# Kernel optimization log

Hardware: AMD Instinct MI355X
Metric: run time of the kernel (lower is better)

## Reference

```python
import jax, jax.numpy as jnp
import numpy as np

N_QUBITS = 12
DIM = 2 ** N_QUBITS
N_RES_LAYERS = 3
N_HEADS = 2
N_ATTN_LAYERS = 2
SEQ_LEN = 64
HORIZON = 4
BATCH = 8
N_PARAMS = N_QUBITS * 2 * N_ATTN_LAYERS  # 48
FEAT = N_QUBITS * N_HEADS  # 24

# ---- static (numpy) precomputed gate structures (little-endian, qiskit convention) ----
_idx = np.arange(DIM)

def _cx_perm(c, t):
    # CNOT: flip target bit where control bit is 1 -> index permutation
    return np.where(((_idx >> c) & 1) == 1, _idx ^ (1 << t), _idx)

def _cz_phase(a, b):
    return (1.0 - 2.0 * (((_idx >> a) & 1) * ((_idx >> b) & 1))).astype(np.float32)

CX_LADDER = [jnp.asarray(_cx_perm(i, i + 1)) for i in range(N_QUBITS - 1)]
CX_RING = jnp.asarray(_cx_perm(N_QUBITS - 1, 0))
CX_LONG = jnp.asarray(_cx_perm(0, N_QUBITS - 1))
_CZ = []
for _layer in range(N_RES_LAYERS):
    _ph = np.ones(DIM, np.float32)
    for _i in range(_layer % 2, N_QUBITS - 1, 2):
        _ph *= _cz_phase(_i, _i + 1)
    _CZ.append(jnp.asarray(_ph))
# Qiskit Pauli label 'I'*i + 'Z' + 'I'*(n-i-1) acts on qubit n-1-i (big-endian labels)
Z_SIGNS = jnp.asarray(np.stack([
    (1.0 - 2.0 * ((_idx >> (N_QUBITS - 1 - i)) & 1)).astype(np.float32)
    for i in range(N_QUBITS)]))  # (n, DIM)


def _apply_1q(state, gate, q):
    # state: (..., DIM); gate: (2,2) or (...,2,2) broadcastable against leading dims
    hi = DIM >> (q + 1)
    lo = 1 << q
    s = state.reshape(state.shape[:-1] + (hi, 2, lo))
    out = jnp.einsum('...ij,...hjl->...hil', gate, s)
    return out.reshape(state.shape)


def _ry(theta):
    c = jnp.cos(theta / 2)
    s = jnp.sin(theta / 2)
    g = jnp.stack([jnp.stack([c, -s], -1), jnp.stack([s, c], -1)], -2)
    return g.astype(jnp.complex64)


def _rz(phi):
    em = jnp.exp(-0.5j * phi)
    ep = jnp.exp(0.5j * phi)
    z = jnp.zeros_like(em)
    return jnp.stack([jnp.stack([em, z], -1), jnp.stack([z, ep], -1)], -2)


def _u3(t, p, l):
    ct = jnp.cos(t / 2).astype(jnp.complex64)
    st = jnp.sin(t / 2).astype(jnp.complex64)
    return jnp.stack([jnp.stack([ct, -jnp.exp(1j * l) * st]),
                      jnp.stack([jnp.exp(1j * p) * st, jnp.exp(1j * (p + l)) * ct])])


def _encode_reservoir(x, res_params):
    # x: (B,T) normalized scalars -> batched statevectors (B,T,DIM)
    B, T = x.shape
    # H^{\otimes n} |0...0> = uniform superposition
    state = jnp.full((B, T, DIM), 1.0 / np.sqrt(DIM), jnp.complex64)
    for i in range(N_QUBITS):
        state = _apply_1q(state, _ry(x * np.pi * (i + 1) / N_QUBITS), i)
        state = _apply_1q(state, _rz(x * np.pi / (i + 1)), i)
    for p in CX_LADDER:
        state = state[..., p]
    state = state[..., CX_RING]
    # fixed random reservoir
    for layer in range(N_RES_LAYERS):
        for i in range(N_QUBITS):
            g = _u3(res_params[layer, i, 0], res_params[layer, i, 1], res_params[layer, i, 2])
            state = _apply_1q(state, g, i)
        state = state * _CZ[layer]
        state = state[..., CX_LONG]  # n > 2
    return state


def _project(state, params):
    # projection circuit: per layer RY/RZ on each qubit then CNOT ladder; then <Z_i>
    for layer in range(N_ATTN_LAYERS):
        for i in range(N_QUBITS):
            k = (layer * N_QUBITS + i) * 2
            state = _apply_1q(state, _ry(params[k]), i)
            state = _apply_1q(state, _rz(params[k + 1]), i)
        for p in CX_LADDER:
            state = state[..., p]
    probs = state.real ** 2 + state.imag ** 2  # (B,T,DIM)
    return jnp.einsum('btd,qd->btq', probs, Z_SIGNS)  # (B,T,n)


def setup_inputs() -> dict:
    key = jax.random.key(0)
    ks = jax.random.split(key, 6)
    sequence = jax.random.uniform(ks[0], (BATCH, SEQ_LEN), jnp.float32)
    res_params = jax.random.uniform(ks[1], (N_RES_LAYERS, N_QUBITS, 3), jnp.float32,
                                    minval=0.0, maxval=2.0 * np.pi)
    head_params = jax.random.uniform(ks[2], (N_HEADS, 3, N_PARAMS), jnp.float32,
                                     minval=0.0, maxval=2.0 * np.pi)
    W1 = jax.random.normal(ks[3], (FEAT, 2 * FEAT), jnp.float32) / np.sqrt(FEAT)
    b1 = jnp.zeros((2 * FEAT,), jnp.float32)
    W2 = jax.random.normal(ks[4], (2 * FEAT, HORIZON), jnp.float32) / np.sqrt(2 * FEAT)
    b2 = jnp.zeros((HORIZON,), jnp.float32)
    return {'sequence': sequence, 'res_params': res_params, 'head_params': head_params,
            'W1': W1, 'b1': b1, 'W2': W2, 'b2': b2}


def reference(sequence, res_params, head_params, W1, b1, W2, b2):
    states = _encode_reservoir(sequence, res_params)  # (B,T,DIM)
    T = sequence.shape[1]
    mask = jnp.triu(jnp.full((T, T), -1e9, jnp.float32), k=1)
    outs = []
    for h in range(N_HEADS):
        Q = _project(states, head_params[h, 0])
        K = _project(states, head_params[h, 1])
        V = _project(states, head_params[h, 2])
        scores = jnp.einsum('btd,bsd->bts', Q, K) / np.sqrt(N_QUBITS) + mask
        attn = jax.nn.softmax(scores, axis=-1)
        outs.append(jnp.einsum('bts,bsd->btd', attn, V))
    feats = jnp.concatenate(outs, -1)  # (B,T,FEAT)
    last = feats[:, -1, :]
    hdn = jax.nn.gelu(last @ W1 + b1, approximate=False)  # torch GELU default = exact erf
    pred = hdn @ W2 + b2  # (B, HORIZON)
    return pred
```

## Files before the change

### kernel.cpp

```cpp
#include <hip/hip_runtime.h>
#include <hip/hip_bf16.h>


#define PADDED 4224

__device__ __forceinline__ int PD(int j) { return j + (j >> 5); }

__device__ __forceinline__ int mapIdx(int j, int mode) {
  if (mode == 1) { int k = j ^ ((j >> 11) & 1); return k ^ ((k & 0x7FF) << 1); }
  if (mode == 2) { return j ^ ((j & 1) << 11); }
  if (mode == 3) { return j ^ ((j & 0x7FF) << 1); }
  return j;
}

template <int L>
__device__ __forceinline__ int layoutIdx(int tid, int r) {
  if constexpr (L == 0) return (tid << 4) | r;
  else if constexpr (L == 1) return ((tid & 0xF0) << 4) | (r << 4) | (tid & 15);
  else return (r << 8) | tid;
}

template <int L>
__device__ __forceinline__ void ldsRead16(const float* sR, const float* sI, int tid, int mode,
                                          float ar[16], float ai[16]) {
#pragma unroll
  for (int r = 0; r < 16; ++r) {
    int j = layoutIdx<L>(tid, r);
    int a = PD(mapIdx(j, mode));
    ar[r] = sR[a]; ai[r] = sI[a];
  }
}

template <int L>
__device__ __forceinline__ void ldsWrite16(float* sR, float* sI, int tid,
                                           const float ar[16], const float ai[16], int czmask) {
#pragma unroll
  for (int r = 0; r < 16; ++r) {
    int j = layoutIdx<L>(tid, r);
    float vr = ar[r], vi = ai[r];
    if (czmask) {
      float sg = (__popc((j & (j >> 1)) & czmask) & 1) ? -1.0f : 1.0f;
      vr *= sg; vi *= sg;
    }
    int a = PD(j);
    sR[a] = vr; sI[a] = vi;
  }
}

__device__ __forceinline__ void applyU34(float ar[16], float ai[16], const float (*ut)[8]) {
#pragma unroll
  for (int b = 0; b < 4; ++b) {
    const float* u = ut[b];
    float u00r = u[0], u00i = u[1], u01r = u[2], u01i = u[3];
    float u10r = u[4], u10i = u[5], u11r = u[6], u11i = u[7];
#pragma unroll
    for (int m = 0; m < 8; ++m) {
      int p0 = ((m >> b) << (b + 1)) | (m & ((1 << b) - 1));
      int p1 = p0 | (1 << b);
      float x0r = ar[p0], x0i = ai[p0], x1r = ar[p1], x1i = ai[p1];
      ar[p0] = u00r * x0r - u00i * x0i + u01r * x1r - u01i * x1i;
      ai[p0] = u00r * x0i + u00i * x0r + u01r * x1i + u01i * x1r;
      ar[p1] = u10r * x0r - u10i * x0i + u11r * x1r - u11i * x1i;
      ai[p1] = u10r * x0i + u10i * x0r + u11r * x1i + u11i * x1r;
    }
  }
}

__device__ __forceinline__ void applyRyRz4(float ar[16], float ai[16], const float4* gt) {
#pragma unroll
  for (int b = 0; b < 4; ++b) {
    float4 g = gt[b];
    float c = g.x, s = g.y, zr = g.z, zi = g.w;
#pragma unroll
    for (int m = 0; m < 8; ++m) {
      int p0 = ((m >> b) << (b + 1)) | (m & ((1 << b) - 1));
      int p1 = p0 | (1 << b);
      float n0r = c * ar[p0] - s * ar[p1];
      float n0i = c * ai[p0] - s * ai[p1];
      float n1r = s * ar[p0] + c * ar[p1];
      float n1i = s * ai[p0] + c * ai[p1];
      ar[p0] = n0r * zr + n0i * zi;  ai[p0] = n0i * zr - n0r * zi;
      ar[p1] = n1r * zr - n1i * zi;  ai[p1] = n1i * zr + n1r * zi;
    }
  }
}

template <int L>
__device__ __forceinline__ void encPass(float* sR, float* sI, int tid, int mode,
                                        const float (*ut)[8], int czmask) {
  float ar[16], ai[16];
  ldsRead16<L>(sR, sI, tid, mode, ar, ai);
  if (mode != 0) __syncthreads();
  applyU34(ar, ai, ut);
  ldsWrite16<L>(sR, sI, tid, ar, ai, czmask);
  __syncthreads();
}

template <int L>
__device__ __forceinline__ void projPass(float* sR, float* sI, int tid, int mode, const float4* gt) {
  float ar[16], ai[16];
  ldsRead16<L>(sR, sI, tid, mode, ar, ai);
  if (mode != 0) __syncthreads();
  applyRyRz4(ar, ai, gt);
  ldsWrite16<L>(sR, sI, tid, ar, ai, 0);
  __syncthreads();
}

__device__ __forceinline__ void projFinal(const float* sR, const float* sI, int tid,
                                          const float4* gt, float feat[12]) {
  float ar[16], ai[16];
#pragma unroll
  for (int r = 0; r < 16; ++r) {
    int a = PD((r << 8) | tid);
    ar[r] = sR[a]; ai[r] = sI[a];
  }
  applyRyRz4(ar, ai, gt);
  float sp = 0.f, f0 = 0.f, f1 = 0.f, f2 = 0.f, f3 = 0.f;
  int pt = __popc(tid) & 1;
#pragma unroll
  for (int r = 0; r < 16; ++r) {
    float p = ar[r] * ar[r] + ai[r] * ai[r];
    sp += p;
    int tr = r ^ (r << 1); tr ^= (tr << 2);
    f0 += ((pt ^ ((tr >> 3) & 1)) ? -p : p);
    f1 += ((pt ^ ((tr >> 2) & 1)) ? -p : p);
    f2 += ((pt ^ ((tr >> 1) & 1)) ? -p : p);
    f3 += ((pt ^ (tr & 1)) ? -p : p);
  }
  feat[0] = f0; feat[1] = f1; feat[2] = f2; feat[3] = f3;
  int tt = tid ^ (tid << 1); tt ^= (tt << 2); tt ^= (tt << 4);
#pragma unroll
  for (int q = 4; q < 12; ++q)
    feat[q] = ((tt >> (11 - q)) & 1) ? -sp : sp;
}

__device__ __forceinline__ float waveReduce(float v) {
#pragma unroll
  for (int off = 32; off; off >>= 1) v += __shfl_xor(v, off, 64);
  return v;
}

__global__ __launch_bounds__(256, 2) void qstates_kernel(
    const float* __restrict__ seq, const float* __restrict__ resp,
    const float* __restrict__ hparams, float* __restrict__ ws) {
  __shared__ float sRe[PADDED], sIm[PADDED];
  __shared__ float4 qtab[12];
  __shared__ float utab[36][8];
  __shared__ float4 ptab[24];
  __shared__ float red[4][12];

  const int tid = threadIdx.x;
  const int blk = blockIdx.x;
  const int b = blk >> 6;
  const int t = blk & 63;
  const float x = seq[(b << 6) | t];
  const float PI = 3.14159265358979323846f;
  const float RS2 = 0.70710678118654752440f;

  if (tid < 12) {
    int i = tid;
    float th = x * PI * (float)(i + 1) / 12.0f;
    float ph = x * PI / (float)(i + 1);
    float s, c;  sincosf(0.5f * th, &s, &c);
    float zi, zr; sincosf(0.5f * ph, &zi, &zr);
    float k0 = (c - s) * RS2, k1 = (c + s) * RS2;
    qtab[i] = make_float4(k0 * zr, -k0 * zi, k1 * zr, k1 * zi);
  }
  if (tid >= 64 && tid < 100) {
    int i = tid - 64;
    const float* rp = resp + i * 3;
    float st, ct;  sincosf(0.5f * rp[0], &st, &ct);
    float sp2, cp; sincosf(rp[1], &sp2, &cp);
    float sl, cl;  sincosf(rp[2], &sl, &cl);
    float spl, cpl; sincosf(rp[1] + rp[2], &spl, &cpl);
    float* u = utab[i];
    u[0] = ct;       u[1] = 0.0f;
    u[2] = -cl * st; u[3] = -sl * st;
    u[4] = cp * st;  u[5] = sp2 * st;
    u[6] = cpl * ct; u[7] = spl * ct;
  }
  __syncthreads();

  {
    float pr, pi;
    {
      float4 g = qtab[4];
      int sb = tid & 1;
      pr = sb ? g.z : g.x; pi = sb ? g.w : g.y;
    }
#pragma unroll
    for (int q = 5; q < 12; ++q) {
      float4 g = qtab[q];
      int sb = (tid >> (q - 4)) & 1;
      float fr = sb ? g.z : g.x, fi = sb ? g.w : g.y;
      float nr = pr * fr - pi * fi;
      pi = pr * fi + pi * fr; pr = nr;
    }
    float4 g0 = qtab[0], g1 = qtab[1], g2 = qtab[2], g3 = qtab[3];
    float c01r[4], c01i[4], c23r[4], c23i[4];
#pragma unroll
    for (int i2 = 0; i2 < 4; ++i2) {
      float f0r = (i2 & 1) ? g0.z : g0.x, f0i = (i2 & 1) ? g0.w : g0.y;
      float f1r = (i2 & 2) ? g1.z : g1.x, f1i = (i2 & 2) ? g1.w : g1.y;
      c01r[i2] = f0r * f1r - f0i * f1i; c01i[i2] = f0r * f1i + f0i * f1r;
      float f2r = (i2 & 1) ? g2.z : g2.x, f2i = (i2 & 1) ? g2.w : g2.y;
      float f3r = (i2 & 2) ? g3.z : g3.x, f3i = (i2 & 2) ? g3.w : g3.y;
      c23r[i2] = f2r * f3r - f2i * f3i; c23i[i2] = f2r * f3i + f2i * f3r;
    }
#pragma unroll
    for (int r = 0; r < 16; ++r) {
      float lr = c01r[r & 3] * c23r[r >> 2] - c01i[r & 3] * c23i[r >> 2];
      float li = c01r[r & 3] * c23i[r >> 2] + c01i[r & 3] * c23r[r >> 2];
      int a = PD((tid << 4) | r);
      sRe[a] = pr * lr - pi * li;
      sIm[a] = pr * li + pi * lr;
    }
  }
  __syncthreads();

  for (int l = 0; l < 3; ++l) {
    int czm = (l & 1) ? 0x2AA : 0x555;
    encPass<0>(sRe, sIm, tid, (l == 0) ? 1 : 2, &utab[l * 12], 0);
    encPass<1>(sRe, sIm, tid, 0, &utab[l * 12 + 4], 0);
    encPass<2>(sRe, sIm, tid, 0, &utab[l * 12 + 8], czm);
  }

  float encR[16], encI[16];
#pragma unroll
  for (int r = 0; r < 16; ++r) {
    int j = (tid << 4) | r;
    int a = PD(j ^ ((j & 1) << 11));
    encR[r] = sRe[a]; encI[r] = sIm[a];
  }

  float* wsK = ws;
  float* wsV = ws + 12288;
  float* wsQ = ws + 24576;

  const int nproj = (t == 63) ? 6 : 4;
  for (int pj = 0; pj < nproj; ++pj) {
    int h, which;
    if (pj < 4) { h = pj >> 1; which = (pj & 1) ? 2 : 1; }
    else        { h = pj - 4;  which = 0; }
    const float* hp = hparams + (h * 3 + which) * 48;
    if (tid < 24) {
      int k = tid * 2;
      float s, c;  sincosf(0.5f * hp[k], &s, &c);
      float zi, zr; sincosf(0.5f * hp[k + 1], &zi, &zr);
      ptab[tid] = make_float4(c, s, zr, zi);
    }
    __syncthreads();

    {
      float ar[16], ai[16];
#pragma unroll
      for (int r = 0; r < 16; ++r) { ar[r] = encR[r]; ai[r] = encI[r]; }
      applyRyRz4(ar, ai, &ptab[0]);
      ldsWrite16<0>(sRe, sIm, tid, ar, ai, 0);
      __syncthreads();
    }
    projPass<1>(sRe, sIm, tid, 0, &ptab[4]);
    projPass<2>(sRe, sIm, tid, 0, &ptab[8]);
    projPass<0>(sRe, sIm, tid, 3, &ptab[12]);
    projPass<1>(sRe, sIm, tid, 0, &ptab[16]);

    float feat[12];
    projFinal(sRe, sIm, tid, &ptab[20], feat);
#pragma unroll
    for (int q = 0; q < 12; ++q) feat[q] = waveReduce(feat[q]);
    int wid = tid >> 6;
    if ((tid & 63) == 0) {
#pragma unroll
      for (int q = 0; q < 12; ++q) red[wid][q] = feat[q];
    }
    __syncthreads();
    if (tid < 12) {
      float v = red[0][tid] + red[1][tid] + red[2][tid] + red[3][tid];
      float* dst;
      if (which == 1)      dst = wsK + (((h << 3) + b) * 64 + t) * 12;
      else if (which == 2) dst = wsV + (((h << 3) + b) * 64 + t) * 12;
      else                 dst = wsQ + ((h << 3) + b) * 12;
      dst[tid] = v;
    }
    __syncthreads();
  }
}

__global__ __launch_bounds__(64) void qhead_kernel(
    const float* __restrict__ ws,
    const float* __restrict__ W1, const float* __restrict__ b1,
    const float* __restrict__ W2, const float* __restrict__ b2,
    float* __restrict__ out) {
  __shared__ float feats[24];
  __shared__ float hdn[48];
  const int b = blockIdx.x;
  const int lane = threadIdx.x;
  const float* Kf = ws;
  const float* Vf = ws + 12288;
  const float* Qf = ws + 24576;
  for (int h = 0; h < 2; ++h) {
    const float* q  = Qf + ((h << 3) + b) * 12;
    const float* kr = Kf + ((((h << 3) + b) << 6) + lane) * 12;
    float dot = 0.f;
#pragma unroll
    for (int d = 0; d < 12; ++d) dot += q[d] * kr[d];
    dot *= 0.288675134594812882f;
    float mx = dot;
#pragma unroll
    for (int off = 32; off; off >>= 1) mx = fmaxf(mx, __shfl_xor(mx, off, 64));
    float e = expf(dot - mx);
    float se = e;
#pragma unroll
    for (int off = 32; off; off >>= 1) se += __shfl_xor(se, off, 64);
    float a = e / se;
    const float* vr = Vf + ((((h << 3) + b) << 6) + lane) * 12;
#pragma unroll
    for (int d = 0; d < 12; ++d) {
      float v = a * vr[d];
#pragma unroll
      for (int off = 32; off; off >>= 1) v += __shfl_xor(v, off, 64);
      if (lane == 0) feats[h * 12 + d] = v;
    }
  }
  __syncthreads();
  if (lane < 48) {
    float acc = b1[lane];
#pragma unroll
    for (int f = 0; f < 24; ++f) acc += feats[f] * W1[f * 48 + lane];
    hdn[lane] = 0.5f * acc * (1.0f + erff(acc * 0.70710678118654752440f));
  }
  __syncthreads();
  if (lane < 4) {
    float acc = b2[lane];
#pragma unroll
    for (int k = 0; k < 48; ++k) acc += hdn[k] * W2[k * 4 + lane];
    out[(b << 2) | lane] = acc;
  }
}

extern "C" void kernel_launch(void* const* d_in, const int* in_sizes, int n_in,
                              void* d_out, int out_size, void* d_ws, size_t ws_size,
                              hipStream_t stream) {
  const float* seq     = (const float*)d_in[0];
  const float* resp    = (const float*)d_in[1];
  const float* hparams = (const float*)d_in[2];
  const float* W1      = (const float*)d_in[3];
  const float* b1      = (const float*)d_in[4];
  const float* W2      = (const float*)d_in[5];
  const float* b2      = (const float*)d_in[6];
  float* out = (float*)d_out;
  float* ws  = (float*)d_ws;

  hipLaunchKernelGGL(qstates_kernel, dim3(512), dim3(256), 0, stream, seq, resp, hparams, ws);
  hipLaunchKernelGGL(qhead_kernel, dim3(8), dim3(64), 0, stream, ws, W1, b1, W2, b2, out);
}
```

Measured before the change: 182.9 us.

## Split encoder and projections into separate kernels to parallelize projections

The fused per-timestep kernel is split in two. An encoder kernel writes each encoded statevector to workspace, and a projection kernel launches one block per (timestep, head, Q/K/V) projection, 2064 blocks instead of 512, so the serial per-block projection loop is spread across the GPU. Gate math is also trimmed: the known-zero u00 imaginary term is dropped from U3, and RZ is applied as a relative phase on the |1> amplitude only. That phase-only form relies on global phase not affecting the Z expectation values. The split path needs about 16 MB of workspace for the statevector round trip through global memory, and it falls back to the monolithic kernel when the workspace is too small.

```diff
diff --git a/kernel.cpp b/kernel.cpp
--- a/kernel.cpp
+++ b/kernel.cpp
@@ -51,15 +51,16 @@
 #pragma unroll
   for (int b = 0; b < 4; ++b) {
     const float* u = ut[b];
-    float u00r = u[0], u00i = u[1], u01r = u[2], u01i = u[3];
+    float u00r = u[0];
+    float u01r = u[2], u01i = u[3];
     float u10r = u[4], u10i = u[5], u11r = u[6], u11i = u[7];
 #pragma unroll
     for (int m = 0; m < 8; ++m) {
       int p0 = ((m >> b) << (b + 1)) | (m & ((1 << b) - 1));
       int p1 = p0 | (1 << b);
       float x0r = ar[p0], x0i = ai[p0], x1r = ar[p1], x1i = ai[p1];
-      ar[p0] = u00r * x0r - u00i * x0i + u01r * x1r - u01i * x1i;
-      ai[p0] = u00r * x0i + u00i * x0r + u01r * x1i + u01i * x1r;
+      ar[p0] = u00r * x0r + u01r * x1r - u01i * x1i;
+      ai[p0] = u00r * x0i + u01r * x1i + u01i * x1r;
       ar[p1] = u10r * x0r - u10i * x0i + u11r * x1r - u11i * x1i;
       ai[p1] = u10r * x0i + u10i * x0r + u11r * x1i + u11i * x1r;
     }
@@ -75,12 +76,13 @@
     for (int m = 0; m < 8; ++m) {
       int p0 = ((m >> b) << (b + 1)) | (m & ((1 << b) - 1));
       int p1 = p0 | (1 << b);
-      float n0r = c * ar[p0] - s * ar[p1];
-      float n0i = c * ai[p0] - s * ai[p1];
-      float n1r = s * ar[p0] + c * ar[p1];
-      float n1i = s * ai[p0] + c * ai[p1];
-      ar[p0] = n0r * zr + n0i * zi;  ai[p0] = n0i * zr - n0r * zi;
-      ar[p1] = n1r * zr - n1i * zi;  ai[p1] = n1i * zr + n1r * zi;
+      float x0r = ar[p0], x0i = ai[p0], x1r = ar[p1], x1i = ai[p1];
+      float n0r = c * x0r - s * x1r;
+      float n0i = c * x0i - s * x1i;
+      float wr  = s * x0r + c * x1r;
+      float wi  = s * x0i + c * x1i;
+      ar[p0] = n0r;              ai[p0] = n0i;
+      ar[p1] = wr * zr - wi * zi; ai[p1] = wr * zi + wi * zr;
     }
   }
 }
@@ -140,23 +142,10 @@
   return v;
 }
 
-__global__ __launch_bounds__(256, 2) void qstates_kernel(
-    const float* __restrict__ seq, const float* __restrict__ resp,
-    const float* __restrict__ hparams, float* __restrict__ ws) {
-  __shared__ float sRe[PADDED], sIm[PADDED];
-  __shared__ float4 qtab[12];
-  __shared__ float utab[36][8];
-  __shared__ float4 ptab[24];
-  __shared__ float red[4][12];
-
-  const int tid = threadIdx.x;
-  const int blk = blockIdx.x;
-  const int b = blk >> 6;
-  const int t = blk & 63;
-  const float x = seq[(b << 6) | t];
+
+__device__ __forceinline__ void buildQtab(float4* qtab, int tid, float x) {
   const float PI = 3.14159265358979323846f;
   const float RS2 = 0.70710678118654752440f;
-
   if (tid < 12) {
     int i = tid;
     float th = x * PI * (float)(i + 1) / 12.0f;
@@ -166,6 +155,9 @@
     float k0 = (c - s) * RS2, k1 = (c + s) * RS2;
     qtab[i] = make_float4(k0 * zr, -k0 * zi, k1 * zr, k1 * zi);
   }
+}
+
+__device__ __forceinline__ void buildUtab(float (*utab)[8], int tid, const float* resp) {
   if (tid >= 64 && tid < 100) {
     int i = tid - 64;
     const float* rp = resp + i * 3;
@@ -179,43 +171,174 @@
     u[4] = cp * st;  u[5] = sp2 * st;
     u[6] = cpl * ct; u[7] = spl * ct;
   }
-  __syncthreads();
-
+}
+
+__device__ __forceinline__ void initProduct(float* sRe, float* sIm, int tid, const float4* qtab) {
+  float pr, pi;
   {
-    float pr, pi;
-    {
-      float4 g = qtab[4];
-      int sb = tid & 1;
-      pr = sb ? g.z : g.x; pi = sb ? g.w : g.y;
-    }
-#pragma unroll
-    for (int q = 5; q < 12; ++q) {
-      float4 g = qtab[q];
-      int sb = (tid >> (q - 4)) & 1;
-      float fr = sb ? g.z : g.x, fi = sb ? g.w : g.y;
-      float nr = pr * fr - pi * fi;
-      pi = pr * fi + pi * fr; pr = nr;
-    }
-    float4 g0 = qtab[0], g1 = qtab[1], g2 = qtab[2], g3 = qtab[3];
-    float c01r[4], c01i[4], c23r[4], c23i[4];
-#pragma unroll
-    for (int i2 = 0; i2 < 4; ++i2) {
-      float f0r = (i2 & 1) ? g0.z : g0.x, f0i = (i2 & 1) ? g0.w : g0.y;
-      float f1r = (i2 & 2) ? g1.z : g1.x, f1i = (i2 & 2) ? g1.w : g1.y;
-      c01r[i2] = f0r * f1r - f0i * f1i; c01i[i2] = f0r * f1i + f0i * f1r;
-      float f2r = (i2 & 1) ? g2.z : g2.x, f2i = (i2 & 1) ? g2.w : g2.y;
-      float f3r = (i2 & 2) ? g3.z : g3.x, f3i = (i2 & 2) ? g3.w : g3.y;
-      c23r[i2] = f2r * f3r - f2i * f3i; c23i[i2] = f2r * f3i + f2i * f3r;
-    }
+    float4 g = qtab[4];
+    int sb = tid & 1;
+    pr = sb ? g.z : g.x; pi = sb ? g.w : g.y;
+  }
+#pragma unroll
+  for (int q = 5; q < 12; ++q) {
+    float4 g = qtab[q];
+    int sb = (tid >> (q - 4)) & 1;
+    float fr = sb ? g.z : g.x, fi = sb ? g.w : g.y;
+    float nr = pr * fr - pi * fi;
+    pi = pr * fi + pi * fr; pr = nr;
+  }
+  float4 g0 = qtab[0], g1 = qtab[1], g2 = qtab[2], g3 = qtab[3];
+  float c01r[4], c01i[4], c23r[4], c23i[4];
+#pragma unroll
+  for (int i2 = 0; i2 < 4; ++i2) {
+    float f0r = (i2 & 1) ? g0.z : g0.x, f0i = (i2 & 1) ? g0.w : g0.y;
+    float f1r = (i2 & 2) ? g1.z : g1.x, f1i = (i2 & 2) ? g1.w : g1.y;
+    c01r[i2] = f0r * f1r - f0i * f1i; c01i[i2] = f0r * f1i + f0i * f1r;
+    float f2r = (i2 & 1) ? g2.z : g2.x, f2i = (i2 & 1) ? g2.w : g2.y;
+    float f3r = (i2 & 2) ? g3.z : g3.x, f3i = (i2 & 2) ? g3.w : g3.y;
+    c23r[i2] = f2r * f3r - f2i * f3i; c23i[i2] = f2r * f3i + f2i * f3r;
+  }
+#pragma unroll
+  for (int r = 0; r < 16; ++r) {
+    float lr = c01r[r & 3] * c23r[r >> 2] - c01i[r & 3] * c23i[r >> 2];
+    float li = c01r[r & 3] * c23i[r >> 2] + c01i[r & 3] * c23r[r >> 2];
+    int a = PD((tid << 4) | r);
+    sRe[a] = pr * lr - pi * li;
+    sIm[a] = pr * li + pi * lr;
+  }
+}
+
+__device__ __forceinline__ void buildPtab(float4* ptab, int tid, const float* hp) {
+  if (tid < 24) {
+    int k = tid * 2;
+    float s, c;  sincosf(0.5f * hp[k], &s, &c);
+    float zi, zr; sincosf(hp[k + 1], &zi, &zr);
+    ptab[tid] = make_float4(c, s, zr, zi);
+  }
+}
+
+
+__global__ __launch_bounds__(256, 2) void enc_kernel(
+    const float* __restrict__ seq, const float* __restrict__ resp,
+    float* __restrict__ wsStates) {
+  __shared__ float sRe[PADDED], sIm[PADDED];
+  __shared__ float4 qtab[12];
+  __shared__ float utab[36][8];
+
+  const int tid = threadIdx.x;
+  const int blk = blockIdx.x;
+  const float x = seq[blk];
+
+  buildQtab(qtab, tid, x);
+  buildUtab(utab, tid, resp);
+  __syncthreads();
+
+  initProduct(sRe, sIm, tid, qtab);
+  __syncthreads();
+
+  encPass<0>(sRe, sIm, tid, 1, &utab[0], 0);
+  encPass<1>(sRe, sIm, tid, 0, &utab[4], 0);
+  encPass<2>(sRe, sIm, tid, 0, &utab[8], 0x555);
+  encPass<0>(sRe, sIm, tid, 2, &utab[12], 0);
+  encPass<1>(sRe, sIm, tid, 0, &utab[16], 0);
+  encPass<2>(sRe, sIm, tid, 0, &utab[20], 0x2AA);
+  encPass<0>(sRe, sIm, tid, 2, &utab[24], 0);
+  encPass<1>(sRe, sIm, tid, 0, &utab[28], 0);
+
+  {
+    float ar[16], ai[16];
+    ldsRead16<2>(sRe, sIm, tid, 0, ar, ai);
+    applyU34(ar, ai, &utab[32]);
+    float* gR = wsStates + (size_t)blk * 8192;
+    float* gI = gR + 4096;
 #pragma unroll
     for (int r = 0; r < 16; ++r) {
-      float lr = c01r[r & 3] * c23r[r >> 2] - c01i[r & 3] * c23i[r >> 2];
-      float li = c01r[r & 3] * c23i[r >> 2] + c01i[r & 3] * c23r[r >> 2];
-      int a = PD((tid << 4) | r);
-      sRe[a] = pr * lr - pi * li;
-      sIm[a] = pr * li + pi * lr;
-    }
-  }
+      int j = (r << 8) | tid;
+      float sg = (__popc((j & (j >> 1)) & 0x555) & 1) ? -1.0f : 1.0f;
+      int g = j ^ ((j & 1) << 11);
+      gR[g] = sg * ar[r];
+      gI[g] = sg * ai[r];
+    }
+  }
+}
+
+__global__ __launch_bounds__(256, 4) void proj_kernel(
+    const float* __restrict__ wsStates, const float* __restrict__ hparams,
+    float* __restrict__ featBase) {
+  __shared__ float sRe[PADDED], sIm[PADDED];
+  __shared__ float4 ptab[24];
+  __shared__ float red[4][12];
+
+  const int tid = threadIdx.x;
+  const int bid = blockIdx.x;
+  int h, which, s;
+  if (bid < 2048) { s = bid >> 2; int pp = bid & 3; h = pp >> 1; which = 1 + (pp & 1); }
+  else            { int i = bid - 2048; h = i & 1; s = (((i >> 1) << 6) | 63); which = 0; }
+  const int b = s >> 6, t = s & 63;
+
+  buildPtab(ptab, tid, hparams + (h * 3 + which) * 48);
+
+  float ar[16], ai[16];
+  const float4* pR = (const float4*)(wsStates + (size_t)s * 8192 + (tid << 4));
+  const float4* pI = (const float4*)(wsStates + (size_t)s * 8192 + 4096 + (tid << 4));
+#pragma unroll
+  for (int k = 0; k < 4; ++k) {
+    float4 vr = pR[k], vi = pI[k];
+    ar[4 * k] = vr.x; ar[4 * k + 1] = vr.y; ar[4 * k + 2] = vr.z; ar[4 * k + 3] = vr.w;
+    ai[4 * k] = vi.x; ai[4 * k + 1] = vi.y; ai[4 * k + 2] = vi.z; ai[4 * k + 3] = vi.w;
+  }
+  __syncthreads();
+
+  applyRyRz4(ar, ai, &ptab[0]);
+  ldsWrite16<0>(sRe, sIm, tid, ar, ai, 0);
+  __syncthreads();
+
+  projPass<1>(sRe, sIm, tid, 0, &ptab[4]);
+  projPass<2>(sRe, sIm, tid, 0, &ptab[8]);
+  projPass<0>(sRe, sIm, tid, 3, &ptab[12]);
+  projPass<1>(sRe, sIm, tid, 0, &ptab[16]);
+
+  float feat[12];
+  projFinal(sRe, sIm, tid, &ptab[20], feat);
+#pragma unroll
+  for (int q = 0; q < 12; ++q) feat[q] = waveReduce(feat[q]);
+  int wid = tid >> 6;
+  if ((tid & 63) == 0) {
+#pragma unroll
+    for (int q = 0; q < 12; ++q) red[wid][q] = feat[q];
+  }
+  __syncthreads();
+  if (tid < 12) {
+    float v = red[0][tid] + red[1][tid] + red[2][tid] + red[3][tid];
+    float* dst;
+    if (which == 1)      dst = featBase + (((h << 3) + b) * 64 + t) * 12;
+    else if (which == 2) dst = featBase + 12288 + (((h << 3) + b) * 64 + t) * 12;
+    else                 dst = featBase + 24576 + ((h << 3) + b) * 12;
+    dst[tid] = v;
+  }
+}
+
+
+__global__ __launch_bounds__(256, 2) void qstates_mono(
+    const float* __restrict__ seq, const float* __restrict__ resp,
+    const float* __restrict__ hparams, float* __restrict__ featBase) {
+  __shared__ float sRe[PADDED], sIm[PADDED];
+  __shared__ float4 qtab[12];
+  __shared__ float utab[36][8];
+  __shared__ float4 ptab[24];
+  __shared__ float red[4][12];
+
+  const int tid = threadIdx.x;
+  const int blk = blockIdx.x;
+  const int b = blk >> 6;
+  const int t = blk & 63;
+  const float x = seq[blk];
+
+  buildQtab(qtab, tid, x);
+  buildUtab(utab, tid, resp);
+  __syncthreads();
+  initProduct(sRe, sIm, tid, qtab);
   __syncthreads();
 
   for (int l = 0; l < 3; ++l) {
@@ -233,32 +356,20 @@
     encR[r] = sRe[a]; encI[r] = sIm[a];
   }
 
-  float* wsK = ws;
-  float* wsV = ws + 12288;
-  float* wsQ = ws + 24576;
-
   const int nproj = (t == 63) ? 6 : 4;
   for (int pj = 0; pj < nproj; ++pj) {
     int h, which;
     if (pj < 4) { h = pj >> 1; which = (pj & 1) ? 2 : 1; }
     else        { h = pj - 4;  which = 0; }
-    const float* hp = hparams + (h * 3 + which) * 48;
-    if (tid < 24) {
-      int k = tid * 2;
-      float s, c;  sincosf(0.5f * hp[k], &s, &c);
-      float zi, zr; sincosf(0.5f * hp[k + 1], &zi, &zr);
-      ptab[tid] = make_float4(c, s, zr, zi);
-    }
+    buildPtab(ptab, tid, hparams + (h * 3 + which) * 48);
     __syncthreads();
 
-    {
-      float ar[16], ai[16];
-#pragma unroll
-      for (int r = 0; r < 16; ++r) { ar[r] = encR[r]; ai[r] = encI[r]; }
-      applyRyRz4(ar, ai, &ptab[0]);
-      ldsWrite16<0>(sRe, sIm, tid, ar, ai, 0);
-      __syncthreads();
-    }
+    float ar[16], ai[16];
+#pragma unroll
+    for (int r = 0; r < 16; ++r) { ar[r] = encR[r]; ai[r] = encI[r]; }
+    applyRyRz4(ar, ai, &ptab[0]);
+    ldsWrite16<0>(sRe, sIm, tid, ar, ai, 0);
+    __syncthreads();
     projPass<1>(sRe, sIm, tid, 0, &ptab[4]);
     projPass<2>(sRe, sIm, tid, 0, &ptab[8]);
     projPass<0>(sRe, sIm, tid, 3, &ptab[12]);
@@ -277,17 +388,18 @@
     if (tid < 12) {
       float v = red[0][tid] + red[1][tid] + red[2][tid] + red[3][tid];
       float* dst;
-      if (which == 1)      dst = wsK + (((h << 3) + b) * 64 + t) * 12;
-      else if (which == 2) dst = wsV + (((h << 3) + b) * 64 + t) * 12;
-      else                 dst = wsQ + ((h << 3) + b) * 12;
+      if (which == 1)      dst = featBase + (((h << 3) + b) * 64 + t) * 12;
+      else if (which == 2) dst = featBase + 12288 + (((h << 3) + b) * 64 + t) * 12;
+      else                 dst = featBase + 24576 + ((h << 3) + b) * 12;
       dst[tid] = v;
     }
     __syncthreads();
   }
 }
 
+
 __global__ __launch_bounds__(64) void qhead_kernel(
-    const float* __restrict__ ws,
+    const float* __restrict__ featBase,
     const float* __restrict__ W1, const float* __restrict__ b1,
     const float* __restrict__ W2, const float* __restrict__ b2,
     float* __restrict__ out) {
@@ -295,9 +407,9 @@
   __shared__ float hdn[48];
   const int b = blockIdx.x;
   const int lane = threadIdx.x;
-  const float* Kf = ws;
-  const float* Vf = ws + 12288;
-  const float* Qf = ws + 24576;
+  const float* Kf = featBase;
+  const float* Vf = featBase + 12288;
+  const float* Qf = featBase + 24576;
   for (int h = 0; h < 2; ++h) {
     const float* q  = Qf + ((h << 3) + b) * 12;
     const float* kr = Kf + ((((h << 3) + b) << 6) + lane) * 12;
@@ -351,6 +463,15 @@
   float* out = (float*)d_out;
   float* ws  = (float*)d_ws;
 
-  hipLaunchKernelGGL(qstates_kernel, dim3(512), dim3(256), 0, stream, seq, resp, hparams, ws);
-  hipLaunchKernelGGL(qhead_kernel, dim3(8), dim3(64), 0, stream, ws, W1, b1, W2, b2, out);
-}
+  const size_t needSplit = ((size_t)512 * 8192 + 24768) * sizeof(float);
+  if (ws_size >= needSplit) {
+    float* wsStates = ws;
+    float* featBase = ws + (size_t)512 * 8192;
+    hipLaunchKernelGGL(enc_kernel, dim3(512), dim3(256), 0, stream, seq, resp, wsStates);
+    hipLaunchKernelGGL(proj_kernel, dim3(2064), dim3(256), 0, stream, wsStates, hparams, featBase);
+    hipLaunchKernelGGL(qhead_kernel, dim3(8), dim3(64), 0, stream, featBase, W1, b1, W2, b2, out);
+  } else {
+    hipLaunchKernelGGL(qstates_mono, dim3(512), dim3(256), 0, stream, seq, resp, hparams, ws);
+    hipLaunchKernelGGL(qhead_kernel, dim3(8), dim3(64), 0, stream, ws, W1, b1, W2, b2, out);
+  }
+}
```

Measured after the change: 147.9 us. -19.1%, faster.
